# Kernel optimization log

Hardware: AMD Instinct MI355X
Metric: run time of the kernel (lower is better)

The kernel has to match this reference:

```python
import jax, jax.numpy as jnp
import numpy as np

BN_EPS = 1e-5


def setup_inputs() -> dict:
    key = jax.random.key(0)
    k1, k2 = jax.random.split(key, 2)
    N_out, K, Cin, Cout = 65536, 8, 256, 512
    N_in = N_out * K
    data = jax.random.normal(k1, (N_in, Cin), dtype=jnp.float32)
    # Kaiming-ish scale for the conv weight [K*Cin, Cout]
    weight = jax.random.normal(k2, (K * Cin, Cout), dtype=jnp.float32) * (1.0 / np.sqrt(K * Cin))
    bias = jnp.zeros((Cout,), dtype=jnp.float32)
    gamma = jnp.ones((Cout,), dtype=jnp.float32)
    beta = jnp.zeros((Cout,), dtype=jnp.float32)
    # Full-octree stride-2 child indices: output node i gathers children 8i..8i+7
    neigh = jnp.arange(N_in, dtype=jnp.int64).reshape(N_out, K)
    return {"data": data, "weight": weight, "bias": bias,
            "gamma": gamma, "beta": beta, "neigh": neigh}


def reference(data, weight, bias, gamma, beta, neigh):
    # OctreeConv (kernel 2x2x2, stride 2, nempty): gather 8 children per output
    # node, then a single GEMM with weight [8*Cin, Cout].
    N_out, K = neigh.shape
    Cin = data.shape[1]
    feat = data[neigh.reshape(-1)].reshape(N_out, K * Cin)  # [N_out, 8*Cin]
    out = feat @ weight + bias                              # [N_out, Cout]
    # BatchNorm1d, training mode: biased batch stats over the node dim.
    mean = jnp.mean(out, axis=0)
    var = jnp.mean(jnp.square(out), axis=0) - jnp.square(mean)
    out = (out - mean) * jax.lax.rsqrt(var + BN_EPS) * gamma + beta
    return out
```

## Files before the change

kernel.cpp:

```cpp
#include <hip/hip_runtime.h>
#include <hip/hip_bf16.h>

typedef __attribute__((ext_vector_type(8))) short bf16x8;
typedef __attribute__((ext_vector_type(4))) float f32x4;

#define N_OUT 65536
#define CIN   256
#define COUT  512
#define BM    128
#define BK    64
#define NKS   32

__device__ __forceinline__ unsigned short f2bf(float f) {
  union { __hip_bfloat16 h; unsigned short u; } c;
  c.h = __float2bfloat16(f);
  return c.u;
}

__device__ __forceinline__ bf16x8 pack8(f32x4 a, f32x4 b) {
  unsigned short u[8];
  u[0] = f2bf(a.x); u[1] = f2bf(a.y); u[2] = f2bf(a.z); u[3] = f2bf(a.w);
  u[4] = f2bf(b.x); u[5] = f2bf(b.y); u[6] = f2bf(b.z); u[7] = f2bf(b.w);
  return *reinterpret_cast<bf16x8*>(u);
}

__device__ __forceinline__ void gload_lds16(const float* g, float* l) {
  __builtin_amdgcn_global_load_lds(
      (const __attribute__((address_space(1))) void*)g,
      (__attribute__((address_space(3))) void*)l, 16, 0, 0);
}

__global__ void wprep_kernel(const float* __restrict__ W, unsigned short* __restrict__ Wt) {
  int idx = blockIdx.x * blockDim.x + threadIdx.x;
  if (idx >= 64 * 4 * COUT) return;
  int n  = idx & (COUT - 1);
  int s  = (idx >> 9) & 3;
  int kb = idx >> 11;
  unsigned short tmp[8];
#pragma unroll
  for (int w = 0; w < 8; ++w)
    tmp[w] = f2bf(W[(size_t)(kb * 32 + s * 8 + w) * COUT + n]);
  *reinterpret_cast<bf16x8*>(Wt + ((size_t)kb * 16384 + n * 32 + s * 8)) =
      *reinterpret_cast<bf16x8*>(tmp);
}

__global__ __launch_bounds__(512, 2) void gemm_kernel(
    const float* __restrict__ data,
    const int*   __restrict__ neigh,
    const unsigned short* __restrict__ Wt,
    float* __restrict__ out,
    float* __restrict__ psum,
    float* __restrict__ psq)
{
  __shared__ union {
    float as[3][BM * BK];
    float st[4][COUT];
  } sm;
  __shared__ unsigned int offs[BM * 8];

  const int tid = threadIdx.x;
  const int l   = tid & 63;
  const int w   = tid >> 6;
  const int wr  = w >> 2;
  const int wc  = w & 3;
  const int lg  = l >> 4;
  const int lm  = l & 15;
  const int m0  = blockIdx.x * BM;

  f32x4 acc[4][8];
#pragma unroll
  for (int i = 0; i < 4; ++i)
#pragma unroll
    for (int j = 0; j < 8; ++j) acc[i][j] = (f32x4){0.f, 0.f, 0.f, 0.f};

  bf16x8 af[4], bfC[8], bfN[8];

  for (int e = tid; e < BM * 8; e += 512)
    offs[e] = ((unsigned)neigh[(size_t)m0 * 8 + e]) << 8;
  __syncthreads();

#define AISSUE(t_, buf_) do { \
    const int cn_ = (t_) >> 2; \
    const int k0_ = ((t_) & 3) * 64; \
    _Pragma("unroll") \
    for (int j_ = 0; j_ < 4; ++j_) { \
      int rg_ = j_ * 4 + (l >> 4); \
      unsigned off_ = offs[(w * 16 + rg_) * 8 + cn_]; \
      const float* src_ = data + off_ + k0_ + (((l & 15) ^ rg_) << 2); \
      float* dst_ = &sm.as[buf_][(w * 16 + j_ * 4) * BK]; \
      gload_lds16(src_, dst_); \
    } \
  } while (0)

#define LOAD_B(kb, bf) do { \
    const unsigned short* wt_ = Wt + (size_t)(kb) * 16384 + wc * 4096 + lm * 32 + lg * 8; \
    _Pragma("unroll") \
    for (int ni_ = 0; ni_ < 8; ++ni_) bf[ni_] = *reinterpret_cast<const bf16x8*>(wt_ + ni_ * 512); \
  } while (0)

#define LOAD_AF(buf_, h_) do { \
    _Pragma("unroll") \
    for (int mi_ = 0; mi_ < 4; ++mi_) { \
      int R_ = wr * 64 + mi_ * 16 + lm; \
      const f32x4* b_ = reinterpret_cast<const f32x4*>(&sm.as[buf_][R_ * BK]); \
      int c0_ = (h_) * 8 + lg * 2; \
      f32x4 x0_ = b_[c0_ ^ (R_ & 15)]; \
      f32x4 x1_ = b_[(c0_ + 1) ^ (R_ & 15)]; \
      af[mi_] = pack8(x0_, x1_); \
    } \
  } while (0)

#define DO_MFMA(bf) do { \
    _Pragma("unroll") \
    for (int mi_ = 0; mi_ < 4; ++mi_) \
      _Pragma("unroll") \
      for (int ni_ = 0; ni_ < 8; ++ni_) \
        acc[mi_][ni_] = __builtin_amdgcn_mfma_f32_16x16x32_bf16(af[mi_], bf[ni_], acc[mi_][ni_], 0, 0, 0); \
  } while (0)

  AISSUE(0, 0);
  AISSUE(1, 1);
  LOAD_B(0, bfC);

  int bufc = 0;
  int bufp = 2;
#pragma unroll 1
  for (int t = 0; t < NKS; ++t) {
    if (t + 2 < NKS) AISSUE(t + 2, bufp);
    LOAD_B(2 * t + 1, bfN);
    asm volatile("s_waitcnt vmcnt(24)" ::: "memory");
    __builtin_amdgcn_s_barrier();
    LOAD_AF(bufc, 0);
    DO_MFMA(bfC);
    if (t + 1 < NKS) LOAD_B(2 * t + 2, bfC);
    LOAD_AF(bufc, 1);
    DO_MFMA(bfN);
    __builtin_amdgcn_s_barrier();
    bufc = (bufc == 2) ? 0 : bufc + 1;
    bufp = (bufp == 2) ? 0 : bufp + 1;
  }

#pragma unroll
  for (int mi = 0; mi < 4; ++mi) {
#pragma unroll
    for (int r = 0; r < 4; ++r) {
      size_t row = (size_t)(m0 + wr * 64 + mi * 16 + lg * 4 + r);
      float* op = out + row * COUT + wc * 128 + lm;
#pragma unroll
      for (int ni = 0; ni < 8; ++ni) op[ni * 16] = acc[mi][ni][r];
    }
  }

  __syncthreads();
#pragma unroll
  for (int ni = 0; ni < 8; ++ni) {
    float s1 = 0.f, s2 = 0.f;
#pragma unroll
    for (int mi = 0; mi < 4; ++mi)
#pragma unroll
      for (int r = 0; r < 4; ++r) { float v = acc[mi][ni][r]; s1 += v; s2 += v * v; }
    s1 += __shfl_xor(s1, 16, 64); s1 += __shfl_xor(s1, 32, 64);
    s2 += __shfl_xor(s2, 16, 64); s2 += __shfl_xor(s2, 32, 64);
    if (l < 16) {
      sm.st[wr][wc * 128 + ni * 16 + l]     = s1;
      sm.st[2 + wr][wc * 128 + ni * 16 + l] = s2;
    }
  }
  __syncthreads();
  {
    float S = sm.st[0][tid] + sm.st[1][tid];
    float Q = sm.st[2][tid] + sm.st[3][tid];
    psum[(size_t)blockIdx.x * COUT + tid] = S;
    psq [(size_t)blockIdx.x * COUT + tid] = Q;
  }
#undef AISSUE
#undef LOAD_B
#undef LOAD_AF
#undef DO_MFMA
}

__global__ void reduce1_kernel(const float* __restrict__ psum, const float* __restrict__ psq,
                               float* __restrict__ p2) {
  int c = threadIdx.x, b = blockIdx.x;
  float s = 0.f, q = 0.f;
#pragma unroll
  for (int j = 0; j < 8; ++j) {
    s += psum[(size_t)(b * 8 + j) * COUT + c];
    q += psq [(size_t)(b * 8 + j) * COUT + c];
  }
  p2[b * 1024 + c] = s;
  p2[b * 1024 + 512 + c] = q;
}

__global__ void reduce2_kernel(const float* __restrict__ p2,
                               const float* __restrict__ gamma,
                               const float* __restrict__ beta,
                               float* __restrict__ scsh) {
  int c = threadIdx.x;
  float s = 0.f, q = 0.f;
  for (int b = 0; b < 64; ++b) { s += p2[b * 1024 + c]; q += p2[b * 1024 + 512 + c]; }
  float mean = s * (1.f / 65536.f);
  float var  = q * (1.f / 65536.f) - mean * mean;
  float rs   = rsqrtf(var + 1e-5f);
  float sc   = gamma[c] * rs;
  scsh[c] = sc;
  scsh[COUT + c] = beta[c] - mean * sc;
}

__global__ void bn_kernel(float* __restrict__ out, const float* __restrict__ scsh) {
  __shared__ float sc[COUT], sh[COUT];
  int t = threadIdx.x;
  sc[t] = scsh[t];
  sh[t] = scsh[COUT + t];
  __syncthreads();
  f32x4* o4 = reinterpret_cast<f32x4*>(out);
  const size_t total  = (size_t)N_OUT * COUT / 4;
  const size_t stride = (size_t)gridDim.x * blockDim.x;
  for (size_t i = (size_t)blockIdx.x * blockDim.x + t; i < total; i += stride) {
    f32x4 v = o4[i];
    int c = ((int)(i & 127)) * 4;
    v.x = v.x * sc[c]     + sh[c];
    v.y = v.y * sc[c + 1] + sh[c + 1];
    v.z = v.z * sc[c + 2] + sh[c + 2];
    v.w = v.w * sc[c + 3] + sh[c + 3];
    o4[i] = v;
  }
}

extern "C" void kernel_launch(void* const* d_in, const int* in_sizes, int n_in,
                              void* d_out, int out_size, void* d_ws, size_t ws_size,
                              hipStream_t stream) {
  const float* data   = (const float*)d_in[0];
  const float* weight = (const float*)d_in[1];
  const float* gamma  = (const float*)d_in[3];
  const float* beta   = (const float*)d_in[4];
  const int*   neigh  = (const int*)d_in[5];
  float* out = (float*)d_out;

  char* ws = (char*)d_ws;
  unsigned short* Wt = (unsigned short*)ws;
  float* psum = (float*)(ws + (2u << 20));
  float* psq  = (float*)(ws + (3u << 20));
  float* p2   = (float*)(ws + (4u << 20));
  float* scsh = (float*)(ws + (4u << 20) + (256u << 10));

  wprep_kernel<<<512, 256, 0, stream>>>(weight, Wt);
  gemm_kernel<<<N_OUT / BM, 512, 0, stream>>>(data, neigh, Wt, out, psum, psq);
  reduce1_kernel<<<64, 512, 0, stream>>>(psum, psq, p2);
  reduce2_kernel<<<1, 512, 0, stream>>>(p2, gamma, beta, scsh);
  bn_kernel<<<2048, 512, 0, stream>>>(out, scsh);
}
```

Measured before the change: 273.6 us.

## Stage weight tiles through LDS with async loads and halve K-step size

```diff
diff --git a/kernel.cpp b/kernel.cpp
--- a/kernel.cpp
+++ b/kernel.cpp
@@ -8,8 +8,8 @@
 #define CIN   256
 #define COUT  512
 #define BM    128
-#define BK    64
-#define NKS   32
+#define BK    32
+#define NKS   64
 
 __device__ __forceinline__ unsigned short f2bf(float f) {
   union { __hip_bfloat16 h; unsigned short u; } c;
@@ -24,7 +24,12 @@
   return *reinterpret_cast<bf16x8*>(u);
 }
 
-__device__ __forceinline__ void gload_lds16(const float* g, float* l) {
+__device__ __forceinline__ void gload_lds16f(const float* g, float* l) {
+  __builtin_amdgcn_global_load_lds(
+      (const __attribute__((address_space(1))) void*)g,
+      (__attribute__((address_space(3))) void*)l, 16, 0, 0);
+}
+__device__ __forceinline__ void gload_lds16u(const unsigned short* g, unsigned short* l) {
   __builtin_amdgcn_global_load_lds(
       (const __attribute__((address_space(1))) void*)g,
       (__attribute__((address_space(3))) void*)l, 16, 0, 0);
@@ -40,7 +45,7 @@
 #pragma unroll
   for (int w = 0; w < 8; ++w)
     tmp[w] = f2bf(W[(size_t)(kb * 32 + s * 8 + w) * COUT + n]);
-  *reinterpret_cast<bf16x8*>(Wt + ((size_t)kb * 16384 + n * 32 + s * 8)) =
+  *reinterpret_cast<bf16x8*>(Wt + ((size_t)kb * 16384 + s * 4096 + n * 8)) =
       *reinterpret_cast<bf16x8*>(tmp);
 }
 
@@ -53,7 +58,10 @@
     float* __restrict__ psq)
 {
   __shared__ union {
-    float as[3][BM * BK];
+    struct {
+      float          a[3][BM * BK];
+      unsigned short b[3][BK * COUT];
+    } r;
     float st[4][COUT];
   } sm;
   __shared__ unsigned int offs[BM * 8];
@@ -73,44 +81,50 @@
 #pragma unroll
     for (int j = 0; j < 8; ++j) acc[i][j] = (f32x4){0.f, 0.f, 0.f, 0.f};
 
-  bf16x8 af[4], bfC[8], bfN[8];
+  bf16x8 af[4], bf[8];
 
   for (int e = tid; e < BM * 8; e += 512)
     offs[e] = ((unsigned)neigh[(size_t)m0 * 8 + e]) << 8;
   __syncthreads();
 
 #define AISSUE(t_, buf_) do { \
-    const int cn_ = (t_) >> 2; \
-    const int k0_ = ((t_) & 3) * 64; \
-    _Pragma("unroll") \
-    for (int j_ = 0; j_ < 4; ++j_) { \
-      int rg_ = j_ * 4 + (l >> 4); \
-      unsigned off_ = offs[(w * 16 + rg_) * 8 + cn_]; \
-      const float* src_ = data + off_ + k0_ + (((l & 15) ^ rg_) << 2); \
-      float* dst_ = &sm.as[buf_][(w * 16 + j_ * 4) * BK]; \
-      gload_lds16(src_, dst_); \
+    const int cn_ = (t_) >> 3; \
+    const int k0_ = ((t_) & 7) * BK; \
+    _Pragma("unroll") \
+    for (int q_ = 0; q_ < 2; ++q_) { \
+      int row_ = w * 16 + q_ * 8 + (l >> 3); \
+      unsigned off_ = offs[row_ * 8 + cn_]; \
+      const float* src_ = data + off_ + k0_ + (((l & 7) ^ ((l >> 3) & 7)) << 2); \
+      gload_lds16f(src_, &sm.r.a[buf_][(w * 16 + q_ * 8) * BK]); \
     } \
   } while (0)
 
-#define LOAD_B(kb, bf) do { \
-    const unsigned short* wt_ = Wt + (size_t)(kb) * 16384 + wc * 4096 + lm * 32 + lg * 8; \
-    _Pragma("unroll") \
-    for (int ni_ = 0; ni_ < 8; ++ni_) bf[ni_] = *reinterpret_cast<const bf16x8*>(wt_ + ni_ * 512); \
-  } while (0)
-
-#define LOAD_AF(buf_, h_) do { \
+#define BISSUE(t_, buf_) do { \
+    const unsigned short* bs_ = Wt + (size_t)(t_) * 16384; \
+    _Pragma("unroll") \
+    for (int p_ = 0; p_ < 4; ++p_) \
+      gload_lds16u(bs_ + (w * 4 + p_) * 512 + l * 8, &sm.r.b[buf_][(w * 4 + p_) * 512]); \
+  } while (0)
+
+#define LOAD_AF(buf_) do { \
     _Pragma("unroll") \
     for (int mi_ = 0; mi_ < 4; ++mi_) { \
       int R_ = wr * 64 + mi_ * 16 + lm; \
-      const f32x4* b_ = reinterpret_cast<const f32x4*>(&sm.as[buf_][R_ * BK]); \
-      int c0_ = (h_) * 8 + lg * 2; \
-      f32x4 x0_ = b_[c0_ ^ (R_ & 15)]; \
-      f32x4 x1_ = b_[(c0_ + 1) ^ (R_ & 15)]; \
+      const f32x4* b_ = reinterpret_cast<const f32x4*>(&sm.r.a[buf_][R_ * BK]); \
+      f32x4 x0_ = b_[(2 * lg)     ^ (R_ & 7)]; \
+      f32x4 x1_ = b_[(2 * lg + 1) ^ (R_ & 7)]; \
       af[mi_] = pack8(x0_, x1_); \
     } \
   } while (0)
 
-#define DO_MFMA(bf) do { \
+#define LOAD_BF(buf_) do { \
+    _Pragma("unroll") \
+    for (int ni_ = 0; ni_ < 8; ++ni_) \
+      bf[ni_] = *reinterpret_cast<const bf16x8*>( \
+          &sm.r.b[buf_][lg * 4096 + (wc * 128 + lm + ni_ * 16) * 8]); \
+  } while (0)
+
+#define DO_MFMA() do { \
     _Pragma("unroll") \
     for (int mi_ = 0; mi_ < 4; ++mi_) \
       _Pragma("unroll") \
@@ -118,27 +132,30 @@
         acc[mi_][ni_] = __builtin_amdgcn_mfma_f32_16x16x32_bf16(af[mi_], bf[ni_], acc[mi_][ni_], 0, 0, 0); \
   } while (0)
 
-  AISSUE(0, 0);
-  AISSUE(1, 1);
-  LOAD_B(0, bfC);
-
-  int bufc = 0;
-  int bufp = 2;
+  BISSUE(0, 0); AISSUE(0, 0);
+  BISSUE(1, 1); AISSUE(1, 1);
+
+  int bufc = 0, bufp = 2;
 #pragma unroll 1
-  for (int t = 0; t < NKS; ++t) {
-    if (t + 2 < NKS) AISSUE(t + 2, bufp);
-    LOAD_B(2 * t + 1, bfN);
-    asm volatile("s_waitcnt vmcnt(24)" ::: "memory");
+  for (int t = 0; t < NKS - 2; ++t) {
+    BISSUE(t + 2, bufp);
+    AISSUE(t + 2, bufp);
+    asm volatile("s_waitcnt vmcnt(12)" ::: "memory");
     __builtin_amdgcn_s_barrier();
-    LOAD_AF(bufc, 0);
-    DO_MFMA(bfC);
-    if (t + 1 < NKS) LOAD_B(2 * t + 2, bfC);
-    LOAD_AF(bufc, 1);
-    DO_MFMA(bfN);
+    LOAD_AF(bufc);
+    LOAD_BF(bufc);
+    DO_MFMA();
     __builtin_amdgcn_s_barrier();
     bufc = (bufc == 2) ? 0 : bufc + 1;
     bufp = (bufp == 2) ? 0 : bufp + 1;
   }
+  asm volatile("s_waitcnt vmcnt(6)" ::: "memory");
+  __builtin_amdgcn_s_barrier();
+  LOAD_AF(bufc); LOAD_BF(bufc); DO_MFMA();
+  bufc = (bufc == 2) ? 0 : bufc + 1;
+  asm volatile("s_waitcnt vmcnt(0)" ::: "memory");
+  __builtin_amdgcn_s_barrier();
+  LOAD_AF(bufc); LOAD_BF(bufc); DO_MFMA();
 
 #pragma unroll
   for (int mi = 0; mi < 4; ++mi) {
@@ -174,8 +191,9 @@
     psq [(size_t)blockIdx.x * COUT + tid] = Q;
   }
 #undef AISSUE
-#undef LOAD_B
+#undef BISSUE
 #undef LOAD_AF
+#undef LOAD_BF
 #undef DO_MFMA
 }
 
```

New measurement: 306.1 us. +11.9%, slower.
